# Kernel tuning notes

Hardware: AMD Instinct MI355X
Metric: run time of the kernel (lower is better)

The kernel has to match this reference:

```python
import jax, jax.numpy as jnp
import numpy as np
from jax import lax


def setup_inputs() -> dict:
    key = jax.random.key(0)
    ks = jax.random.split(key, 6)
    num_u, num_v, num_h, batch = 64, 256, 256, 8192
    # lecun_normal: std = 1/sqrt(fan_in) where fan_in is the last dim
    def lecun(k, shape):
        return jax.random.normal(k, shape, dtype=jnp.float32) * jnp.sqrt(1.0 / shape[1])
    return {
        "u_state": (jax.random.uniform(ks[0], (batch, num_u)) < 0.5).astype(jnp.float32),
        "weights_vu": lecun(ks[1], (num_v, num_u)),
        "weights_hu": lecun(ks[2], (num_h, num_u)),
        "weights_hv": lecun(ks[3], (num_h, num_v)),
        "bias_v": jax.random.normal(ks[4], (num_v,), dtype=jnp.float32) * 0.01,
        "bias_h": jax.random.normal(ks[5], (num_h,), dtype=jnp.float32) * 0.01,
        "therm_steps": 24,
        "size": 8,
    }


def reference(u_state, weights_vu, weights_hu, weights_hv, bias_v, bias_h,
              therm_steps, size):
    """ConditionalRBM.sample: init visible from u, thermalize therm_steps
    Gibbs sweeps, then collect `size` consecutive Gibbs samples."""
    key = jax.random.key(1)

    def bern(k, p):
        # binomial(n=1, p) == bernoulli(p)
        return (jax.random.uniform(k, p.shape) < p).astype(jnp.float32)

    def gibbs_step(v, k):
        k1, k2 = jax.random.split(k)
        ph = jax.nn.sigmoid(v @ weights_hv.T + u_state @ weights_hu.T + bias_h)  # [B,H]
        h = bern(k1, ph)
        pv = jax.nn.sigmoid(h @ weights_hv + u_state @ weights_vu.T + bias_v)    # [B,V]
        return bern(k2, pv)

    ks = jax.random.split(key, therm_steps + size + 1)
    # initial visible state from the conditional prior p(v|u)
    v0 = bern(ks[0], jax.nn.sigmoid(u_state @ weights_vu.T + bias_v))
    # thermalization chain (sequential, loop-carried)
    v_therm, _ = lax.scan(lambda v, k: (gibbs_step(v, k), None), v0, ks[1:1 + therm_steps])
    # sampling chain, stack the `size` samples
    def sample_step(v, k):
        v_new = gibbs_step(v, k)
        return v_new, v_new
    _, samples = lax.scan(sample_step, v_therm, ks[1 + therm_steps:])
    return samples.astype(jnp.uint8)  # [size, B, V]
```

## Files before the change

### kernel.cpp

```cpp
#include <hip/hip_runtime.h>
#include <cstdint>
#include <cstddef>


#pragma clang fp contract(off)

#define BATCH 8192
#define NU 64
#define NF 256
#define RPB 16
#define CH 16
#define NCH (NF / CH)
#define RTI 16
#define THERM 24
#define NSAMP 8
#define NSTEP (THERM + NSAMP)

__host__ __device__ __forceinline__ void tf2x32(uint32_t k0, uint32_t k1,
                                                uint32_t x0, uint32_t x1,
                                                uint32_t* o0, uint32_t* o1) {
  uint32_t ks2 = k0 ^ k1 ^ 0x1BD11BDAu;
  x0 += k0; x1 += k1;
#define TFR(r) { x0 += x1; x1 = (x1 << (r)) | (x1 >> (32 - (r))); x1 ^= x0; }
  TFR(13) TFR(15) TFR(26) TFR(6)
  x0 += k1;  x1 += ks2 + 1u;
  TFR(17) TFR(29) TFR(16) TFR(24)
  x0 += ks2; x1 += k0 + 2u;
  TFR(13) TFR(15) TFR(26) TFR(6)
  x0 += k0;  x1 += k1 + 3u;
  TFR(17) TFR(29) TFR(16) TFR(24)
  x0 += k1;  x1 += ks2 + 4u;
  TFR(13) TFR(15) TFR(26) TFR(6)
  x0 += ks2; x1 += k0 + 5u;
#undef TFR
  *o0 = x0; *o1 = x1;
}

__device__ __forceinline__ float xla_expf(float x) {
  float xc = fminf(x, 88.3762626647950f);
  xc = fmaxf(xc, -88.3762626647949f);
  float fx = floorf(__builtin_fmaf(xc, 1.44269504088896341f, 0.5f));
  float tmp = 0.693359375f * fx;
  float z = -2.12194440e-4f * fx;
  float r = xc - tmp;
  r = r - z;
  z = r * r;
  float y = __builtin_fmaf(r, 1.9875691500e-4f, 1.3981999507e-3f);
  y = __builtin_fmaf(y, r, 8.3334519073e-3f);
  y = __builtin_fmaf(y, r, 4.1665795894e-2f);
  y = __builtin_fmaf(y, r, 1.6666665459e-1f);
  y = __builtin_fmaf(y, r, 5.0000001201e-1f);
  y = __builtin_fmaf(y, z, r);
  y = y + 1.0f;
  int n = (int)fx;
  float p2 = __int_as_float((n + 127) << 23);
  float res = y * p2;
  return fmaxf(res, x);
}

__device__ __forceinline__ float sigmoid_ref(float x) {
  float e = xla_expf(-x);
  return 1.0f / (1.0f + e);
}

__device__ __forceinline__ float bern_sample(uint32_t key0, uint32_t key1,
                                             uint32_t idx, float p) {
  uint32_t b0, b1;
  tf2x32(key0, key1, 0u, idx, &b0, &b1);
  uint32_t bits = b0 ^ b1;
  float u = __uint_as_float((bits >> 9) | 0x3f800000u) - 1.0f;
  return (u < p) ? 1.0f : 0.0f;
}

__device__ __forceinline__ void gld_lds16(const float* g, float* l) {
  __builtin_amdgcn_global_load_lds(
      (const __attribute__((address_space(1))) void*)g,
      (__attribute__((address_space(3))) void*)l, 16, 0, 0);
}

__global__ void k_transpose(const float* __restrict__ Whv,
                            float* __restrict__ WhvT) {
  int j = threadIdx.x;
  int k = blockIdx.x;
  WhvT[k * NF + j] = Whv[j * NF + k];
}

__global__ __launch_bounds__(256, 2) void k_udot(const float* __restrict__ U,
                                                 const float* __restrict__ W,
                                                 float* __restrict__ out) {
  __shared__ __align__(16) float Ulds[NU * RTI];
  const int j = threadIdx.x;
  const int i0 = blockIdx.x * RTI;
  const int si = j & 15;
  const int sg = j >> 4;
  {
    float4 u4 = *(const float4*)(U + (size_t)(i0 + si) * NU + sg * 4);
    Ulds[(sg * 4 + 0) * RTI + si] = u4.x;
    Ulds[(sg * 4 + 1) * RTI + si] = u4.y;
    Ulds[(sg * 4 + 2) * RTI + si] = u4.z;
    Ulds[(sg * 4 + 3) * RTI + si] = u4.w;
  }
  float wreg[NU];
  const float4* wr4 = (const float4*)(W + (size_t)j * NU);
#pragma unroll
  for (int r = 0; r < NU / 4; ++r) {
    float4 t = wr4[r];
    wreg[4 * r + 0] = t.x; wreg[4 * r + 1] = t.y;
    wreg[4 * r + 2] = t.z; wreg[4 * r + 3] = t.w;
  }
  __syncthreads();
  float acc[RTI];
#pragma unroll
  for (int i = 0; i < RTI; ++i) acc[i] = 0.0f;
#pragma unroll
  for (int kk = 0; kk < NU; ++kk) {
    const float w = wreg[kk];
    const float4 s0 = *(const float4*)(&Ulds[kk * RTI + 0]);
    const float4 s1 = *(const float4*)(&Ulds[kk * RTI + 4]);
    const float4 s2 = *(const float4*)(&Ulds[kk * RTI + 8]);
    const float4 s3 = *(const float4*)(&Ulds[kk * RTI + 12]);
    acc[0]  = __builtin_fmaf(s0.x, w, acc[0]);
    acc[1]  = __builtin_fmaf(s0.y, w, acc[1]);
    acc[2]  = __builtin_fmaf(s0.z, w, acc[2]);
    acc[3]  = __builtin_fmaf(s0.w, w, acc[3]);
    acc[4]  = __builtin_fmaf(s1.x, w, acc[4]);
    acc[5]  = __builtin_fmaf(s1.y, w, acc[5]);
    acc[6]  = __builtin_fmaf(s1.z, w, acc[6]);
    acc[7]  = __builtin_fmaf(s1.w, w, acc[7]);
    acc[8]  = __builtin_fmaf(s2.x, w, acc[8]);
    acc[9]  = __builtin_fmaf(s2.y, w, acc[9]);
    acc[10] = __builtin_fmaf(s2.z, w, acc[10]);
    acc[11] = __builtin_fmaf(s2.w, w, acc[11]);
    acc[12] = __builtin_fmaf(s3.x, w, acc[12]);
    acc[13] = __builtin_fmaf(s3.y, w, acc[13]);
    acc[14] = __builtin_fmaf(s3.z, w, acc[14]);
    acc[15] = __builtin_fmaf(s3.w, w, acc[15]);
  }
#pragma unroll
  for (int i = 0; i < RTI; ++i)
    out[(size_t)(i0 + i) * NF + j] = acc[i];
}

__global__ __launch_bounds__(256, 2) void k_chain(
    const float* __restrict__ Whv, const float* __restrict__ WhvT,
    const float* __restrict__ uh, const float* __restrict__ uv,
    const float* __restrict__ bh, const float* __restrict__ bv,
    int* __restrict__ out) {
  __shared__ __align__(16) float Wbuf[2][CH * NF];
  __shared__ __align__(16) float Cu[2][RPB * NF];
  __shared__ uint32_t bitsL[2][RPB * 8];
  __shared__ uint32_t nib[RPB * 64];
  __shared__ float biasL[2][NF];
  __shared__ uint32_t ksL[66];
  __shared__ uint32_t keysL[NSTEP * 4];

  const int t = threadIdx.x;
  const int rowbase = blockIdx.x * RPB;
  const int rg = t >> 6;
  const int cgg = t & 63;
  const int jc = cgg * 4;

  {
    const float4* gu = (const float4*)(uh + (size_t)rowbase * NF);
    const float4* gv = (const float4*)(uv + (size_t)rowbase * NF);
    float4* lu = (float4*)Cu[0];
    float4* lv = (float4*)Cu[1];
#pragma unroll
    for (int q = 0; q < 4; ++q) {
      lu[q * 256 + t] = gu[q * 256 + t];
      lv[q * 256 + t] = gv[q * 256 + t];
    }
    biasL[0][t] = bh[t];
    biasL[1][t] = bv[t];
    if (t < 33) tf2x32(0u, 1u, 0u, (uint32_t)t, &ksL[2 * t], &ksL[2 * t + 1]);
  }
  __syncthreads();
  if (t < NSTEP) {
    uint32_t a = ksL[2 * (1 + t)], b2 = ksL[2 * (1 + t) + 1];
    tf2x32(a, b2, 0u, 0u, &keysL[4 * t + 0], &keysL[4 * t + 1]);
    tf2x32(a, b2, 0u, 1u, &keysL[4 * t + 2], &keysL[4 * t + 3]);
  }
  __syncthreads();

  {
    const uint32_t k0 = ksL[0], k1 = ksL[1];
#pragma unroll
    for (int ri = 0; ri < 4; ++ri) {
      const int lr = rg * 4 + ri;
      const int row = rowbase + lr;
      uint32_t nb = 0;
#pragma unroll
      for (int ci = 0; ci < 4; ++ci) {
        const int j = jc + ci;
        const float x = Cu[1][lr * NF + j] + biasL[1][j];
        const float v = bern_sample(k0, k1, (uint32_t)(row * NF + j),
                                    sigmoid_ref(x));
        nb |= (v != 0.0f ? 1u : 0u) << ci;
      }
      nib[lr * 64 + cgg] = nb;
    }
  }
  __syncthreads();
  if (t < 128) {
    const int lr = t >> 3, wo = t & 7;
    const uint32_t* nn = &nib[lr * 64 + wo * 8];
    uint32_t wrd = 0;
#pragma unroll
    for (int g = 0; g < 8; ++g) wrd |= nn[g] << (4 * g);
    bitsL[0][lr * 8 + wo] = wrd;
  }
  __syncthreads();

#pragma unroll 1
  for (int tt = 0; tt < NSTEP; ++tt) {
#pragma unroll 1
    for (int ph = 0; ph < 2; ++ph) {
      const float* M = ph ? Whv : WhvT;
      const uint32_t* sb = bitsL[ph];
      uint32_t* db = bitsL[ph ^ 1];
      const float* Cl = Cu[ph];
      const float* bl = biasL[ph];
      const uint32_t k0 = keysL[4 * tt + 2 * ph + 0];
      const uint32_t k1 = keysL[4 * tt + 2 * ph + 1];
      int* smp = (ph == 1 && tt >= THERM)
                     ? out + (size_t)(tt - THERM) * BATCH * NF
                     : (int*)nullptr;

      float acc[16];
#pragma unroll
      for (int q = 0; q < 16; ++q) acc[q] = 0.0f;

#pragma unroll
      for (int q = 0; q < 4; ++q)
        gld_lds16(M + (size_t)(q * 256 + t) * 4, &Wbuf[0][(q * 256 + t) * 4]);
      __syncthreads();

#pragma unroll 1
      for (int c = 0; c < NCH; ++c) {
        if (c + 1 < NCH) {
          const float* src = M + (size_t)(c + 1) * CH * NF;
          float* dst = Wbuf[(c + 1) & 1];
#pragma unroll
          for (int q = 0; q < 4; ++q)
            gld_lds16(src + (size_t)(q * 256 + t) * 4,
                      &dst[(q * 256 + t) * 4]);
        }
        const int wi = c >> 1;
        const int hs = (c & 1) * 16;
        const uint32_t wd0 =
            __builtin_amdgcn_readfirstlane(sb[(rg * 4 + 0) * 8 + wi]) >> hs;
        const uint32_t wd1 =
            __builtin_amdgcn_readfirstlane(sb[(rg * 4 + 1) * 8 + wi]) >> hs;
        const uint32_t wd2 =
            __builtin_amdgcn_readfirstlane(sb[(rg * 4 + 2) * 8 + wi]) >> hs;
        const uint32_t wd3 =
            __builtin_amdgcn_readfirstlane(sb[(rg * 4 + 3) * 8 + wi]) >> hs;
        const float* wl = &Wbuf[c & 1][jc];
#pragma unroll
        for (int kk = 0; kk < CH; ++kk) {
          const float4 w = *(const float4*)(wl + kk * NF);
          const float s0 = (wd0 & (1u << kk)) ? 1.0f : 0.0f;
          const float s1 = (wd1 & (1u << kk)) ? 1.0f : 0.0f;
          const float s2 = (wd2 & (1u << kk)) ? 1.0f : 0.0f;
          const float s3 = (wd3 & (1u << kk)) ? 1.0f : 0.0f;
          acc[0]  = __builtin_fmaf(s0, w.x, acc[0]);
          acc[1]  = __builtin_fmaf(s0, w.y, acc[1]);
          acc[2]  = __builtin_fmaf(s0, w.z, acc[2]);
          acc[3]  = __builtin_fmaf(s0, w.w, acc[3]);
          acc[4]  = __builtin_fmaf(s1, w.x, acc[4]);
          acc[5]  = __builtin_fmaf(s1, w.y, acc[5]);
          acc[6]  = __builtin_fmaf(s1, w.z, acc[6]);
          acc[7]  = __builtin_fmaf(s1, w.w, acc[7]);
          acc[8]  = __builtin_fmaf(s2, w.x, acc[8]);
          acc[9]  = __builtin_fmaf(s2, w.y, acc[9]);
          acc[10] = __builtin_fmaf(s2, w.z, acc[10]);
          acc[11] = __builtin_fmaf(s2, w.w, acc[11]);
          acc[12] = __builtin_fmaf(s3, w.x, acc[12]);
          acc[13] = __builtin_fmaf(s3, w.y, acc[13]);
          acc[14] = __builtin_fmaf(s3, w.z, acc[14]);
          acc[15] = __builtin_fmaf(s3, w.w, acc[15]);
        }
        __syncthreads();
      }

      const float4 b4 = *(const float4*)(bl + jc);
#pragma unroll
      for (int ri = 0; ri < 4; ++ri) {
        const int lr = rg * 4 + ri;
        const int row = rowbase + lr;
        const float4 c4 = *(const float4*)(Cl + lr * NF + jc);
        const uint32_t idx0 = (uint32_t)(row * NF + jc);
        const float v0 = bern_sample(k0, k1, idx0 + 0,
            sigmoid_ref((acc[ri * 4 + 0] + c4.x) + b4.x));
        const float v1 = bern_sample(k0, k1, idx0 + 1,
            sigmoid_ref((acc[ri * 4 + 1] + c4.y) + b4.y));
        const float v2 = bern_sample(k0, k1, idx0 + 2,
            sigmoid_ref((acc[ri * 4 + 2] + c4.z) + b4.z));
        const float v3 = bern_sample(k0, k1, idx0 + 3,
            sigmoid_ref((acc[ri * 4 + 3] + c4.w) + b4.w));
        nib[lr * 64 + cgg] = (v0 != 0.0f ? 1u : 0u) |
                             (v1 != 0.0f ? 2u : 0u) |
                             (v2 != 0.0f ? 4u : 0u) |
                             (v3 != 0.0f ? 8u : 0u);
        if (smp) {
          int4 o;
          o.x = (v0 != 0.0f) ? 1 : 0;
          o.y = (v1 != 0.0f) ? 1 : 0;
          o.z = (v2 != 0.0f) ? 1 : 0;
          o.w = (v3 != 0.0f) ? 1 : 0;
          *(int4*)(smp + (size_t)row * NF + jc) = o;
        }
      }
      __syncthreads();
      if (t < 128) {
        const int lr = t >> 3, wo = t & 7;
        const uint32_t* nn = &nib[lr * 64 + wo * 8];
        uint32_t wrd = 0;
#pragma unroll
        for (int g = 0; g < 8; ++g) wrd |= nn[g] << (4 * g);
        db[lr * 8 + wo] = wrd;
      }
      __syncthreads();
    }
  }
}

extern "C" void kernel_launch(void* const* d_in, const int* in_sizes, int n_in,
                              void* d_out, int out_size, void* d_ws, size_t ws_size,
                              hipStream_t stream) {
  const float* u_state = (const float*)d_in[0];
  const float* Wvu     = (const float*)d_in[1];
  const float* Whu     = (const float*)d_in[2];
  const float* Whv     = (const float*)d_in[3];
  const float* bv      = (const float*)d_in[4];
  const float* bh      = (const float*)d_in[5];
  int* out = (int*)d_out;

  float* ws   = (float*)d_ws;
  float* WhvT = ws;
  float* uh   = WhvT + NF * NF;
  float* uv   = uh + (size_t)BATCH * NF;

  k_transpose<<<NF, NF, 0, stream>>>(Whv, WhvT);
  k_udot<<<BATCH / RTI, NF, 0, stream>>>(u_state, Whu, uh);
  k_udot<<<BATCH / RTI, NF, 0, stream>>>(u_state, Wvu, uv);
  k_chain<<<BATCH / RPB, NF, 0, stream>>>(Whv, WhvT, uh, uv, bh, bv, out);

  (void)in_sizes; (void)n_in; (void)out_size; (void)ws_size;
}
```

Baseline: 1.571 ms.

## Double threads per block in chain kernel and keep u-projections in registers

Raises the chain kernel from 256 to 512 threads per block, so each thread handles 2 rows instead of 4 and needs 8 accumulators instead of 16. The per-row u·W projections now live in registers instead of a shared-memory buffer, which frees LDS and registers so more blocks can be resident. The aim is more occupancy and latency hiding on the weight streaming. In exchange each weight value read from LDS feeds half as many FMAs, and synchronisation now spans a larger block.

```diff
diff --git a/kernel.cpp b/kernel.cpp
--- a/kernel.cpp
+++ b/kernel.cpp
@@ -9,6 +9,7 @@
 #define NU 64
 #define NF 256
 #define RPB 16
+#define TPB 512
 #define CH 16
 #define NCH (NF / CH)
 #define RTI 16
@@ -141,13 +142,12 @@
     out[(size_t)(i0 + i) * NF + j] = acc[i];
 }
 
-__global__ __launch_bounds__(256, 2) void k_chain(
+__global__ __launch_bounds__(TPB, 4) void k_chain(
     const float* __restrict__ Whv, const float* __restrict__ WhvT,
     const float* __restrict__ uh, const float* __restrict__ uv,
     const float* __restrict__ bh, const float* __restrict__ bv,
     int* __restrict__ out) {
   __shared__ __align__(16) float Wbuf[2][CH * NF];
-  __shared__ __align__(16) float Cu[2][RPB * NF];
   __shared__ uint32_t bitsL[2][RPB * 8];
   __shared__ uint32_t nib[RPB * 64];
   __shared__ float biasL[2][NF];
@@ -160,20 +160,19 @@
   const int cgg = t & 63;
   const int jc = cgg * 4;
 
-  {
-    const float4* gu = (const float4*)(uh + (size_t)rowbase * NF);
-    const float4* gv = (const float4*)(uv + (size_t)rowbase * NF);
-    float4* lu = (float4*)Cu[0];
-    float4* lv = (float4*)Cu[1];
-#pragma unroll
-    for (int q = 0; q < 4; ++q) {
-      lu[q * 256 + t] = gu[q * 256 + t];
-      lv[q * 256 + t] = gv[q * 256 + t];
-    }
+  float4 cuh[2], cuv[2];
+#pragma unroll
+  for (int ri = 0; ri < 2; ++ri) {
+    const int lr = rg * 2 + ri;
+    cuh[ri] = *(const float4*)(uh + (size_t)(rowbase + lr) * NF + jc);
+    cuv[ri] = *(const float4*)(uv + (size_t)(rowbase + lr) * NF + jc);
+  }
+
+  if (t < NF) {
     biasL[0][t] = bh[t];
     biasL[1][t] = bv[t];
-    if (t < 33) tf2x32(0u, 1u, 0u, (uint32_t)t, &ksL[2 * t], &ksL[2 * t + 1]);
-  }
+  }
+  if (t < 33) tf2x32(0u, 1u, 0u, (uint32_t)t, &ksL[2 * t], &ksL[2 * t + 1]);
   __syncthreads();
   if (t < NSTEP) {
     uint32_t a = ksL[2 * (1 + t)], b2 = ksL[2 * (1 + t) + 1];
@@ -185,18 +184,20 @@
   {
     const uint32_t k0 = ksL[0], k1 = ksL[1];
 #pragma unroll
-    for (int ri = 0; ri < 4; ++ri) {
-      const int lr = rg * 4 + ri;
+    for (int ri = 0; ri < 2; ++ri) {
+      const int lr = rg * 2 + ri;
       const int row = rowbase + lr;
+      const float4 b4 = *(const float4*)(&biasL[1][jc]);
+      const uint32_t idx0 = (uint32_t)(row * NF + jc);
       uint32_t nb = 0;
-#pragma unroll
-      for (int ci = 0; ci < 4; ++ci) {
-        const int j = jc + ci;
-        const float x = Cu[1][lr * NF + j] + biasL[1][j];
-        const float v = bern_sample(k0, k1, (uint32_t)(row * NF + j),
-                                    sigmoid_ref(x));
-        nb |= (v != 0.0f ? 1u : 0u) << ci;
-      }
+      nb |= (bern_sample(k0, k1, idx0 + 0,
+                 sigmoid_ref(cuv[ri].x + b4.x)) != 0.0f ? 1u : 0u);
+      nb |= (bern_sample(k0, k1, idx0 + 1,
+                 sigmoid_ref(cuv[ri].y + b4.y)) != 0.0f ? 2u : 0u);
+      nb |= (bern_sample(k0, k1, idx0 + 2,
+                 sigmoid_ref(cuv[ri].z + b4.z)) != 0.0f ? 4u : 0u);
+      nb |= (bern_sample(k0, k1, idx0 + 3,
+                 sigmoid_ref(cuv[ri].w + b4.w)) != 0.0f ? 8u : 0u);
       nib[lr * 64 + cgg] = nb;
     }
   }
@@ -218,7 +219,6 @@
       const float* M = ph ? Whv : WhvT;
       const uint32_t* sb = bitsL[ph];
       uint32_t* db = bitsL[ph ^ 1];
-      const float* Cl = Cu[ph];
       const float* bl = biasL[ph];
       const uint32_t k0 = keysL[4 * tt + 2 * ph + 0];
       const uint32_t k1 = keysL[4 * tt + 2 * ph + 1];
@@ -226,13 +226,13 @@
                      ? out + (size_t)(tt - THERM) * BATCH * NF
                      : (int*)nullptr;
 
-      float acc[16];
-#pragma unroll
-      for (int q = 0; q < 16; ++q) acc[q] = 0.0f;
-
-#pragma unroll
-      for (int q = 0; q < 4; ++q)
-        gld_lds16(M + (size_t)(q * 256 + t) * 4, &Wbuf[0][(q * 256 + t) * 4]);
+      float acc[8];
+#pragma unroll
+      for (int q = 0; q < 8; ++q) acc[q] = 0.0f;
+
+#pragma unroll
+      for (int q = 0; q < 2; ++q)
+        gld_lds16(M + (size_t)(q * TPB + t) * 4, &Wbuf[0][(q * TPB + t) * 4]);
       __syncthreads();
 
 #pragma unroll 1
@@ -241,54 +241,40 @@
           const float* src = M + (size_t)(c + 1) * CH * NF;
           float* dst = Wbuf[(c + 1) & 1];
 #pragma unroll
-          for (int q = 0; q < 4; ++q)
-            gld_lds16(src + (size_t)(q * 256 + t) * 4,
-                      &dst[(q * 256 + t) * 4]);
+          for (int q = 0; q < 2; ++q)
+            gld_lds16(src + (size_t)(q * TPB + t) * 4,
+                      &dst[(q * TPB + t) * 4]);
         }
         const int wi = c >> 1;
         const int hs = (c & 1) * 16;
         const uint32_t wd0 =
-            __builtin_amdgcn_readfirstlane(sb[(rg * 4 + 0) * 8 + wi]) >> hs;
+            __builtin_amdgcn_readfirstlane(sb[(rg * 2 + 0) * 8 + wi]) >> hs;
         const uint32_t wd1 =
-            __builtin_amdgcn_readfirstlane(sb[(rg * 4 + 1) * 8 + wi]) >> hs;
-        const uint32_t wd2 =
-            __builtin_amdgcn_readfirstlane(sb[(rg * 4 + 2) * 8 + wi]) >> hs;
-        const uint32_t wd3 =
-            __builtin_amdgcn_readfirstlane(sb[(rg * 4 + 3) * 8 + wi]) >> hs;
+            __builtin_amdgcn_readfirstlane(sb[(rg * 2 + 1) * 8 + wi]) >> hs;
         const float* wl = &Wbuf[c & 1][jc];
 #pragma unroll
         for (int kk = 0; kk < CH; ++kk) {
           const float4 w = *(const float4*)(wl + kk * NF);
           const float s0 = (wd0 & (1u << kk)) ? 1.0f : 0.0f;
           const float s1 = (wd1 & (1u << kk)) ? 1.0f : 0.0f;
-          const float s2 = (wd2 & (1u << kk)) ? 1.0f : 0.0f;
-          const float s3 = (wd3 & (1u << kk)) ? 1.0f : 0.0f;
-          acc[0]  = __builtin_fmaf(s0, w.x, acc[0]);
-          acc[1]  = __builtin_fmaf(s0, w.y, acc[1]);
-          acc[2]  = __builtin_fmaf(s0, w.z, acc[2]);
-          acc[3]  = __builtin_fmaf(s0, w.w, acc[3]);
-          acc[4]  = __builtin_fmaf(s1, w.x, acc[4]);
-          acc[5]  = __builtin_fmaf(s1, w.y, acc[5]);
-          acc[6]  = __builtin_fmaf(s1, w.z, acc[6]);
-          acc[7]  = __builtin_fmaf(s1, w.w, acc[7]);
-          acc[8]  = __builtin_fmaf(s2, w.x, acc[8]);
-          acc[9]  = __builtin_fmaf(s2, w.y, acc[9]);
-          acc[10] = __builtin_fmaf(s2, w.z, acc[10]);
-          acc[11] = __builtin_fmaf(s2, w.w, acc[11]);
-          acc[12] = __builtin_fmaf(s3, w.x, acc[12]);
-          acc[13] = __builtin_fmaf(s3, w.y, acc[13]);
-          acc[14] = __builtin_fmaf(s3, w.z, acc[14]);
-          acc[15] = __builtin_fmaf(s3, w.w, acc[15]);
+          acc[0] = __builtin_fmaf(s0, w.x, acc[0]);
+          acc[1] = __builtin_fmaf(s0, w.y, acc[1]);
+          acc[2] = __builtin_fmaf(s0, w.z, acc[2]);
+          acc[3] = __builtin_fmaf(s0, w.w, acc[3]);
+          acc[4] = __builtin_fmaf(s1, w.x, acc[4]);
+          acc[5] = __builtin_fmaf(s1, w.y, acc[5]);
+          acc[6] = __builtin_fmaf(s1, w.z, acc[6]);
+          acc[7] = __builtin_fmaf(s1, w.w, acc[7]);
         }
         __syncthreads();
       }
 
       const float4 b4 = *(const float4*)(bl + jc);
 #pragma unroll
-      for (int ri = 0; ri < 4; ++ri) {
-        const int lr = rg * 4 + ri;
+      for (int ri = 0; ri < 2; ++ri) {
+        const int lr = rg * 2 + ri;
         const int row = rowbase + lr;
-        const float4 c4 = *(const float4*)(Cl + lr * NF + jc);
+        const float4 c4 = ph ? cuv[ri] : cuh[ri];
         const uint32_t idx0 = (uint32_t)(row * NF + jc);
         const float v0 = bern_sample(k0, k1, idx0 + 0,
             sigmoid_ref((acc[ri * 4 + 0] + c4.x) + b4.x));
@@ -344,7 +330,7 @@
   k_transpose<<<NF, NF, 0, stream>>>(Whv, WhvT);
   k_udot<<<BATCH / RTI, NF, 0, stream>>>(u_state, Whu, uh);
   k_udot<<<BATCH / RTI, NF, 0, stream>>>(u_state, Wvu, uv);
-  k_chain<<<BATCH / RPB, NF, 0, stream>>>(Whv, WhvT, uh, uv, bh, bv, out);
+  k_chain<<<BATCH / RPB, TPB, 0, stream>>>(Whv, WhvT, uh, uv, bh, bv, out);
 
   (void)in_sizes; (void)n_in; (void)out_size; (void)ws_size;
 }
```

Result: faster. 1.503 ms (-4.3%).
